# Kernel tuning notes

Measured on AMD Instinct MI355X. Metric: run time of the kernel, lower is better.

## Reference

```python
import jax, jax.numpy as jnp
import numpy as np

N_NODES, N_EDGES = 1024, 4096
D_NODE, D_EDGE, HEADS, N_CLASSES = 128, 256, 4, 16


def setup_inputs() -> dict:
    key = jax.random.key(0)
    ks = jax.random.split(key, 32)
    def w(i, shape):
        return jax.random.normal(ks[i], shape, dtype=jnp.float32) * 0.02
    inp = {
        'node_features': jax.random.normal(ks[0], (N_NODES, D_NODE), dtype=jnp.float32),
        'edge_features': jax.random.normal(ks[1], (N_EDGES, D_EDGE), dtype=jnp.float32),
        'edge_index': jax.random.randint(ks[2], (2, N_EDGES), 0, N_NODES, dtype=jnp.int32),
    }
    i = 3
    for pre in ('a1', 'a2'):
        for nm, shape in [('Wn', (2 * D_NODE, D_EDGE)), ('Wq', (D_EDGE, D_EDGE)),
                          ('Wk', (D_EDGE, D_EDGE)), ('Wv', (D_EDGE, D_EDGE)), ('Wo', (D_EDGE, D_EDGE))]:
            inp[f'{pre}_{nm}'] = w(i, shape); i += 1
            inp[f'{pre}_b{nm[1:].lower()}'] = jnp.zeros((shape[1],), jnp.float32)
    inp['cls_W1'] = w(i, (D_EDGE, D_EDGE)); i += 1
    inp['cls_b1'] = jnp.zeros((D_EDGE,), jnp.float32)
    inp['cls_W2'] = w(i, (D_EDGE, N_CLASSES)); i += 1
    inp['cls_b2'] = jnp.zeros((N_CLASSES,), jnp.float32)
    return inp


def _edge_adjacency(edge_index):
    # edges adjacent iff they share an endpoint (hops=1). [E,E] bool
    src, dst = edge_index[0], edge_index[1]
    return ((src[:, None] == src[None, :]) | (src[:, None] == dst[None, :]) |
            (dst[:, None] == src[None, :]) | (dst[:, None] == dst[None, :]))


def _edge_attention(ef, nf, edge_index, adj, Wn, bn, Wq, bq, Wk, bk, Wv, bv, Wo, bo):
    src, dst = edge_index[0], edge_index[1]
    # gather endpoint node features and fuse into edge representation
    ctx = jnp.concatenate([nf[src], nf[dst]], axis=-1) @ Wn + bn  # [E, D_EDGE]
    x = ef + ctx
    E, D = x.shape
    hd = D // HEADS
    q = (x @ Wq + bq).reshape(E, HEADS, hd)
    k = (x @ Wk + bk).reshape(E, HEADS, hd)
    v = (x @ Wv + bv).reshape(E, HEADS, hd)
    scores = jnp.einsum('ehd,fhd->hef', q, k) / np.float32(np.sqrt(hd))  # [H,E,E]
    scores = jnp.where(adj[None, :, :], scores, jnp.float32(-1e9))
    attn = jax.nn.softmax(scores, axis=-1)
    out = jnp.einsum('hef,fhd->ehd', attn, v).reshape(E, D)
    return x + out @ Wo + bo


def reference(node_features, edge_features, edge_index,
              a1_Wn, a1_bn, a1_Wq, a1_bq, a1_Wk, a1_bk, a1_Wv, a1_bv, a1_Wo, a1_bo,
              a2_Wn, a2_bn, a2_Wq, a2_bq, a2_Wk, a2_bk, a2_Wv, a2_bv, a2_Wo, a2_bo,
              cls_W1, cls_b1, cls_W2, cls_b2):
    adj = _edge_adjacency(edge_index)
    ef = _edge_attention(edge_features, node_features, edge_index, adj,
                         a1_Wn, a1_bn, a1_Wq, a1_bq, a1_Wk, a1_bk, a1_Wv, a1_bv, a1_Wo, a1_bo)
    ef = _edge_attention(ef, node_features, edge_index, adj,
                         a2_Wn, a2_bn, a2_Wq, a2_bq, a2_Wk, a2_bk, a2_Wv, a2_bv, a2_Wo, a2_bo)
    h = jax.nn.gelu(ef @ cls_W1 + cls_b1, approximate=False)
    return h @ cls_W2 + cls_b2
```

## Files before the change

### kernel.cpp

```cpp
#include <hip/hip_runtime.h>
#include <math.h>

#define E_EDGES 4096
#define N_NODES 1024
#define D_NODE 128
#define D_EDGE 256
#define HEADS 4
#define HD 64
#define N_CLASSES 16
#define CAP 128

typedef __attribute__((ext_vector_type(8))) short short8v;
typedef __attribute__((ext_vector_type(4))) short short4v;
typedef __attribute__((ext_vector_type(4))) float f32x4;

__device__ __forceinline__ unsigned short f2bf(float f) {
    unsigned u = __float_as_uint(f);
    return (unsigned short)((u + 0x7FFFu + ((u >> 16) & 1u)) >> 16);
}
__device__ __forceinline__ float bf2f(unsigned short b) {
    return __uint_as_float(((unsigned)b) << 16);
}

__device__ __forceinline__ void gload_lds16(const void* g, void* l) {
    __builtin_amdgcn_global_load_lds((const __attribute__((address_space(1))) void*)g,
                                     (__attribute__((address_space(3))) void*)l, 16, 0, 0);
}

__device__ __forceinline__ void split_unit(
    char* smem, const float* __restrict__ W, short* __restrict__ ho,
    short* __restrict__ lo, int tile)
{
    float* tl = (float*)smem;
    const int t = threadIdx.x;
    const int k0 = (tile >> 2) * 64, n0 = (tile & 3) * 64;
#pragma unroll
    for (int p = 0; p < 4; ++p) {
        const int kr = (t >> 4) + p * 16;
        const int nc = (t & 15) * 4;
        *(float4*)&tl[kr * 65 + nc] = *(const float4*)&W[(size_t)(k0 + kr) * 256 + n0 + nc];
    }
    __syncthreads();
    const int n = t >> 2, ks = (t & 3) * 16;
    short8v h0, h1, l0, l1;
#pragma unroll
    for (int j = 0; j < 8; ++j) {
        const float x = tl[(ks + j) * 65 + n];
        const unsigned short hb = f2bf(x);
        h0[j] = (short)hb; l0[j] = (short)f2bf(x - bf2f(hb));
    }
#pragma unroll
    for (int j = 0; j < 8; ++j) {
        const float x = tl[(ks + 8 + j) * 65 + n];
        const unsigned short hb = f2bf(x);
        h1[j] = (short)hb; l1[j] = (short)f2bf(x - bf2f(hb));
    }
    *(short8v*)&ho[(size_t)(n0 + n) * 256 + k0 + ks] = h0;
    *(short8v*)&ho[(size_t)(n0 + n) * 256 + k0 + ks + 8] = h1;
    *(short8v*)&lo[(size_t)(n0 + n) * 256 + k0 + ks] = l0;
    *(short8v*)&lo[(size_t)(n0 + n) * 256 + k0 + ks + 8] = l1;
}

__device__ __forceinline__ void adj_unit(
    const int* __restrict__ src, const int* __restrict__ dst,
    int* __restrict__ cand, int* __restrict__ ccount, int e, int lane)
{
    const int a = src[e], b = dst[e];
    int* my = cand + (size_t)e * CAP;
    int base = 0;
    for (int c0 = 0; c0 < E_EDGES; c0 += 64) {
        const int f = c0 + lane;
        const int sf = src[f], df = dst[f];
        const bool adj = (sf == a) | (sf == b) | (df == a) | (df == b);
        const unsigned long long mk = __ballot(adj);
        if (adj) {
            const int pos = base + __popcll(mk & ((1ull << lane) - 1ull));
            if (pos < CAP) my[pos] = f;
        }
        base += __popcll(mk);
    }
    if (lane == 0) ccount[e] = (base < CAP) ? base : CAP;
}

__device__ __forceinline__ void mcore32(
    char* smem,
    const float* __restrict__ A, const float* __restrict__ A2,
    const short* __restrict__ BhiT, const short* __restrict__ BloT,
    const float* __restrict__ bias, const float* __restrict__ res,
    const float* __restrict__ res2, float* __restrict__ C,
    int m0, int n0,
    const float* __restrict__ nf, const int* __restrict__ src,
    const int* __restrict__ dst, int act)
{
    short* AsH = (short*)smem;
    short* AsL = (short*)(smem + 5120);
    short* BsH = (short*)(smem + 10240);
    short* BsL = (short*)(smem + 18432);
    const int t = threadIdx.x;
    const int w = t >> 6, lane = t & 63, lr = lane & 15, lg = lane >> 4;
    const int WR = (w >> 1) * 16, WC = (w & 1) * 32;
    const int ar = t >> 3, akc = (t & 7) * 4;
    const int bn = t >> 2, bkc = (t & 3) * 8;

    int nS = 0, nD = 0;
    if (nf) { nS = src[m0 + ar]; nD = dst[m0 + ar]; }

    f32x4 acc0 = {0.f, 0.f, 0.f, 0.f}, acc1 = {0.f, 0.f, 0.f, 0.f};
    float4 av;

#define LOADA_R(k0)                                                            \
    do {                                                                       \
        const int kq = (k0) + akc;                                             \
        if (nf) {                                                              \
            const float* pp = (kq < D_NODE)                                    \
                ? &nf[(size_t)nS * D_NODE + kq]                                \
                : &nf[(size_t)nD * D_NODE + kq - D_NODE];                      \
            av = *(const float4*)pp;                                           \
        } else {                                                               \
            av = *(const float4*)&A[(size_t)(m0 + ar) * 256 + kq];             \
            if (A2) {                                                          \
                const float4 c_ = *(const float4*)&A2[(size_t)(m0 + ar) * 256 + kq]; \
                av.x += c_.x; av.y += c_.y; av.z += c_.z; av.w += c_.w;        \
            }                                                                  \
        }                                                                      \
    } while (0)
#define STOREA_S(buf)                                                          \
    do {                                                                       \
        short4v ah, al;                                                        \
        const float fv[4] = {av.x, av.y, av.z, av.w};                          \
        _Pragma("unroll") for (int j = 0; j < 4; ++j) {                        \
            const unsigned short hb = f2bf(fv[j]);                             \
            ah[j] = (short)hb; al[j] = (short)f2bf(fv[j] - bf2f(hb));          \
        }                                                                      \
        *(short4v*)&AsH[(buf) * 1280 + ar * 40 + akc] = ah;                    \
        *(short4v*)&AsL[(buf) * 1280 + ar * 40 + akc] = al;                    \
    } while (0)
#define STAGE_B(buf, k0)                                                       \
    do {                                                                       \
        gload_lds16(&BhiT[(size_t)(n0 + bn) * 256 + (k0) + bkc],               \
                    BsH + (buf) * 2048 + t * 8);                               \
        gload_lds16(&BloT[(size_t)(n0 + bn) * 256 + (k0) + bkc],               \
                    BsL + (buf) * 2048 + t * 8);                               \
    } while (0)
#define MFMA_STEP(buf)                                                         \
    do {                                                                       \
        const int c0 = WC + lr, c1 = WC + 16 + lr;                             \
        const short8v bH0 = *(const short8v*)&BsH[(buf) * 2048 + c0 * 32 + lg * 8]; \
        const short8v bL0 = *(const short8v*)&BsL[(buf) * 2048 + c0 * 32 + lg * 8]; \
        const short8v bH1 = *(const short8v*)&BsH[(buf) * 2048 + c1 * 32 + lg * 8]; \
        const short8v bL1 = *(const short8v*)&BsL[(buf) * 2048 + c1 * 32 + lg * 8]; \
        const short8v aH = *(const short8v*)&AsH[(buf) * 1280 + (WR + lr) * 40 + lg * 8]; \
        const short8v aL = *(const short8v*)&AsL[(buf) * 1280 + (WR + lr) * 40 + lg * 8]; \
        acc0 = __builtin_amdgcn_mfma_f32_16x16x32_bf16(aH, bH0, acc0, 0, 0, 0);\
        acc1 = __builtin_amdgcn_mfma_f32_16x16x32_bf16(aH, bH1, acc1, 0, 0, 0);\
        acc0 = __builtin_amdgcn_mfma_f32_16x16x32_bf16(aH, bL0, acc0, 0, 0, 0);\
        acc1 = __builtin_amdgcn_mfma_f32_16x16x32_bf16(aH, bL1, acc1, 0, 0, 0);\
        acc0 = __builtin_amdgcn_mfma_f32_16x16x32_bf16(aL, bH0, acc0, 0, 0, 0);\
        acc1 = __builtin_amdgcn_mfma_f32_16x16x32_bf16(aL, bH1, acc1, 0, 0, 0);\
    } while (0)

    LOADA_R(0);
    STAGE_B(0, 0);
    STOREA_S(0);
    __syncthreads();

    for (int kt = 0; kt < 8; ++kt) {
        const int cur = kt & 1;
        if (kt < 7) {
            STAGE_B(cur ^ 1, (kt + 1) * 32);
            LOADA_R((kt + 1) * 32);
        }
        MFMA_STEP(cur);
        if (kt < 7) STOREA_S(cur ^ 1);
        __syncthreads();
    }

#define EPI(accv, ct)                                                          \
    do {                                                                       \
        const int col = n0 + WC + (ct) * 16 + lr;                              \
        const float bb = bias ? bias[col] : 0.f;                               \
        _Pragma("unroll") for (int i = 0; i < 4; ++i) {                        \
            const int row = m0 + WR + lg * 4 + i;                              \
            float v = accv[i] + bb;                                            \
            if (res)  v += res[(size_t)row * D_EDGE + col];                    \
            if (res2) v += res2[(size_t)row * D_EDGE + col];                   \
            if (act == 1) v = 0.5f * v * (1.f + erff(v * 0.70710678118654752f)); \
            C[(size_t)row * D_EDGE + col] = v;                                 \
        }                                                                      \
    } while (0)
    EPI(acc0, 0); EPI(acc1, 1);
#undef LOADA_R
#undef STOREA_S
#undef STAGE_B
#undef MFMA_STEP
#undef EPI
}

__global__ __launch_bounds__(256) void adj_prep(
    const int* __restrict__ src, const int* __restrict__ dst,
    int* __restrict__ cand, int* __restrict__ ccount,
    const float* Wn1, const float* Wn2, short* hiT, short* loT)
{
    __shared__ __attribute__((aligned(16))) char smem[16640];
    if (blockIdx.x < 1024) {
        const int t = threadIdx.x;
        adj_unit(src, dst, cand, ccount, blockIdx.x * 4 + (t >> 6), t & 63);
    } else {
        const int u = blockIdx.x - 1024;
        const int mat = (u >> 4) ? 5 : 0;
        split_unit(smem, (u >> 4) ? Wn2 : Wn1,
                   hiT + (size_t)mat * 65536, loT + (size_t)mat * 65536, u & 15);
    }
}

__global__ __launch_bounds__(256) void ctx_prep(
    const float* __restrict__ nf, const int* __restrict__ src,
    const int* __restrict__ dst, short* hiT, short* loT,
    const float* __restrict__ bn1, const float* __restrict__ bn2,
    float* __restrict__ ctx,
    const float* Wq1, const float* Wk1, const float* Wv1, const float* Wo1,
    const float* Wq2, const float* Wk2, const float* Wv2, const float* Wo2,
    const float* Wc1)
{
    __shared__ __attribute__((aligned(16))) char smem[26624];
    if (blockIdx.x < 1024) {
        const int lid = blockIdx.x;
        const int g = lid & 7, s = lid >> 3;
        const int rowt = g * 32 + (s >> 2);
        const int ct = s & 3;
        const int R = rowt * 32;
        const int Lyr = R >> 12;
        const int r = R & (E_EDGES - 1);
        mcore32(smem, nullptr, nullptr,
                hiT + (size_t)(Lyr * 5) * 65536, loT + (size_t)(Lyr * 5) * 65536,
                Lyr ? bn2 : bn1, nullptr, nullptr,
                ctx + (size_t)Lyr * E_EDGES * D_EDGE,
                r, ct * 64, nf, src, dst, 0);
    } else {
        const int u = blockIdx.x - 1024;
        const int mi = u >> 4;
        const int matIdx[9] = {1, 2, 3, 4, 6, 7, 8, 9, 10};
        const float* Ws[9] = {Wq1, Wk1, Wv1, Wo1, Wq2, Wk2, Wv2, Wo2, Wc1};
        const int mat = matIdx[mi];
        split_unit(smem, Ws[mi], hiT + (size_t)mat * 65536,
                   loT + (size_t)mat * 65536, u & 15);
    }
}

__global__ __launch_bounds__(256) void gemm_qkv32(
    const float* __restrict__ ef_in, const float* __restrict__ ctx,
    const short* __restrict__ whiT, const short* __restrict__ wloT,
    const float* __restrict__ bq, const float* __restrict__ bk,
    const float* __restrict__ bv,
    float* __restrict__ qb, float* __restrict__ kb, float* __restrict__ vb,
    int wbase)
{
    __shared__ __attribute__((aligned(16))) char smem[26624];
    const int lid = blockIdx.x;
    const int g = lid & 7, s = lid >> 3;
    const int rowt = g * 16 + s / 12;
    const int rem = s % 12, wsel = rem >> 2, ct = rem & 3;
    const short* BH = whiT + (size_t)(wbase + 1 + wsel) * 65536;
    const short* BL = wloT + (size_t)(wbase + 1 + wsel) * 65536;
    const float* bias = (wsel == 0) ? bq : (wsel == 1) ? bk : bv;
    float* C = (wsel == 0) ? qb : (wsel == 1) ? kb : vb;
    mcore32(smem, ef_in, ctx, BH, BL, bias, nullptr, nullptr, C,
            rowt * 32, ct * 64, nullptr, nullptr, nullptr, 0);
}

__global__ __launch_bounds__(256) void gemm_g32(
    const float* __restrict__ A, const short* __restrict__ BhiT,
    const short* __restrict__ BloT, const float* __restrict__ bias,
    const float* __restrict__ res, const float* __restrict__ res2,
    float* __restrict__ C, int act)
{
    __shared__ __attribute__((aligned(16))) char smem[26624];
    const int lid = blockIdx.x;
    const int g = lid & 7, s = lid >> 3;
    const int rowt = g * 16 + (s >> 2);
    const int ct = s & 3;
    mcore32(smem, A, nullptr, BhiT, BloT, bias, res, res2, C,
            rowt * 32, ct * 64, nullptr, nullptr, nullptr, act);
}

__global__ __launch_bounds__(256) void attn_sparse5(
    const float* __restrict__ q, const float* __restrict__ k,
    const float* __restrict__ v, const int* __restrict__ cand,
    const int* __restrict__ ccount, float* __restrict__ out)
{
    __shared__ int lc[4][CAP];
    const int t = threadIdx.x;
    const int w = t >> 6, lane = t & 63;
    const int e = blockIdx.x * 4 + w;
    const int h = lane >> 4, il = lane & 15;
    const int m = ccount[e];
    for (int i = lane; i < m; i += 64) lc[w][i] = cand[(size_t)e * CAP + i];

    const float4 q4 = *(const float4*)&q[(size_t)e * D_EDGE + h * HD + il * 4];
    float M = -1e30f, L = 0.f;
    float4 O = make_float4(0.f, 0.f, 0.f, 0.f);

    int i = 0;
    for (; i + 2 <= m; i += 2) {
        const int f0 = lc[w][i], f1 = lc[w][i + 1];
        const float4 k0 = *(const float4*)&k[(size_t)f0 * D_EDGE + h * HD + il * 4];
        const float4 v0 = *(const float4*)&v[(size_t)f0 * D_EDGE + h * HD + il * 4];
        const float4 k1 = *(const float4*)&k[(size_t)f1 * D_EDGE + h * HD + il * 4];
        const float4 v1 = *(const float4*)&v[(size_t)f1 * D_EDGE + h * HD + il * 4];
        float s0 = q4.x * k0.x + q4.y * k0.y + q4.z * k0.z + q4.w * k0.w;
        float s1 = q4.x * k1.x + q4.y * k1.y + q4.z * k1.z + q4.w * k1.w;
        s0 += __shfl_xor(s0, 1); s1 += __shfl_xor(s1, 1);
        s0 += __shfl_xor(s0, 2); s1 += __shfl_xor(s1, 2);
        s0 += __shfl_xor(s0, 4); s1 += __shfl_xor(s1, 4);
        s0 += __shfl_xor(s0, 8); s1 += __shfl_xor(s1, 8);
        s0 *= 0.125f; s1 *= 0.125f;
        const float Mn = fmaxf(M, fmaxf(s0, s1));
        const float al = __expf(M - Mn);
        const float p0 = __expf(s0 - Mn), p1 = __expf(s1 - Mn);
        O.x = O.x * al + p0 * v0.x + p1 * v1.x;
        O.y = O.y * al + p0 * v0.y + p1 * v1.y;
        O.z = O.z * al + p0 * v0.z + p1 * v1.z;
        O.w = O.w * al + p0 * v0.w + p1 * v1.w;
        L = L * al + p0 + p1;
        M = Mn;
    }
    if (i < m) {
        const int f = lc[w][i];
        const float4 kv = *(const float4*)&k[(size_t)f * D_EDGE + h * HD + il * 4];
        const float4 vv = *(const float4*)&v[(size_t)f * D_EDGE + h * HD + il * 4];
        float s = q4.x * kv.x + q4.y * kv.y + q4.z * kv.z + q4.w * kv.w;
        s += __shfl_xor(s, 1);
        s += __shfl_xor(s, 2);
        s += __shfl_xor(s, 4);
        s += __shfl_xor(s, 8);
        s *= 0.125f;
        const float Mn = fmaxf(M, s);
        const float al = __expf(M - Mn);
        const float p = __expf(s - Mn);
        O.x = O.x * al + p * vv.x;
        O.y = O.y * al + p * vv.y;
        O.z = O.z * al + p * vv.z;
        O.w = O.w * al + p * vv.w;
        L = L * al + p;
        M = Mn;
    }
    const float invL = 1.f / L;
    float4 r = make_float4(O.x * invL, O.y * invL, O.z * invL, O.w * invL);
    *(float4*)&out[(size_t)e * D_EDGE + h * HD + il * 4] = r;
}

__global__ __launch_bounds__(256) void cls_out(
    const float* __restrict__ h, const float* __restrict__ W2,
    const float* __restrict__ b2, float* __restrict__ outp)
{
    __shared__ __attribute__((aligned(16))) float W2s[256 * 16];
    const int t = threadIdx.x;
    const int w = t >> 6, lane = t & 63, lr = lane & 15, lg = lane >> 4;
    const int m0 = blockIdx.x * 16;
#pragma unroll
    for (int p = 0; p < 4; ++p) {
        const int idx = t + 256 * p;
        gload_lds16(&W2[(size_t)idx * 4], W2s + (size_t)idx * 4);
    }
    __syncthreads();
    if (w == 0) {
        f32x4 o = {0.f, 0.f, 0.f, 0.f};
#pragma unroll
        for (int kk = 0; kk < 8; ++kk) {
            const float4 h0 = *(const float4*)&h[(size_t)(m0 + lr) * 256 + kk * 32 + lg * 8];
            const float4 h1 = *(const float4*)&h[(size_t)(m0 + lr) * 256 + kk * 32 + lg * 8 + 4];
            short8v aH, aL;
            const float fv[8] = {h0.x, h0.y, h0.z, h0.w, h1.x, h1.y, h1.z, h1.w};
#pragma unroll
            for (int j = 0; j < 8; ++j) {
                const unsigned short hb = f2bf(fv[j]);
                aH[j] = (short)hb; aL[j] = (short)f2bf(fv[j] - bf2f(hb));
            }
            short8v bH, bL;
#pragma unroll
            for (int j = 0; j < 8; ++j) {
                const float x = W2s[(size_t)(kk * 32 + lg * 8 + j) * 16 + lr];
                const unsigned short hb = f2bf(x);
                bH[j] = (short)hb; bL[j] = (short)f2bf(x - bf2f(hb));
            }
            o = __builtin_amdgcn_mfma_f32_16x16x32_bf16(aH, bH, o, 0, 0, 0);
            o = __builtin_amdgcn_mfma_f32_16x16x32_bf16(aH, bL, o, 0, 0, 0);
            o = __builtin_amdgcn_mfma_f32_16x16x32_bf16(aL, bH, o, 0, 0, 0);
        }
#pragma unroll
        for (int i = 0; i < 4; ++i) {
            const int row = m0 + lg * 4 + i;
            outp[(size_t)row * 16 + lr] = o[i] + b2[lr];
        }
    }
}

extern "C" void kernel_launch(void* const* d_in, const int* in_sizes, int n_in,
                              void* d_out, int out_size, void* d_ws, size_t ws_size,
                              hipStream_t stream)
{
    const float* nf = (const float*)d_in[0];
    const float* ef = (const float*)d_in[1];
    const int* ei = (const int*)d_in[2];
    const int* src = ei;
    const int* dst = ei + E_EDGES;

    const float* a_Wn[2] = {(const float*)d_in[3],  (const float*)d_in[13]};
    const float* a_bn[2] = {(const float*)d_in[4],  (const float*)d_in[14]};
    const float* a_Wq[2] = {(const float*)d_in[5],  (const float*)d_in[15]};
    const float* a_bq[2] = {(const float*)d_in[6],  (const float*)d_in[16]};
    const float* a_Wk[2] = {(const float*)d_in[7],  (const float*)d_in[17]};
    const float* a_bk[2] = {(const float*)d_in[8],  (const float*)d_in[18]};
    const float* a_Wv[2] = {(const float*)d_in[9],  (const float*)d_in[19]};
    const float* a_bv[2] = {(const float*)d_in[10], (const float*)d_in[20]};
    const float* a_Wo[2] = {(const float*)d_in[11], (const float*)d_in[21]};
    const float* a_bo[2] = {(const float*)d_in[12], (const float*)d_in[22]};
    const float* cls_W1 = (const float*)d_in[23];
    const float* cls_b1 = (const float*)d_in[24];
    const float* cls_W2 = (const float*)d_in[25];
    const float* cls_b2 = (const float*)d_in[26];

    const size_t buf = (size_t)E_EDGES * D_EDGE;
    float* ws = (float*)d_ws;
    float* ctx1 = ws + 0 * buf;
    float* ctx2 = ws + 1 * buf;
    float* qb   = ws + 2 * buf;
    float* kb   = ws + 3 * buf;
    float* vb   = ws + 4 * buf;
    float* ao   = ws + 5 * buf;
    float* y1   = ws + 6 * buf;
    float* y2   = ctx1;
    float* hb   = qb;
    int* cand   = (int*)(ws + 7 * buf);
    int* ccount = cand + (size_t)E_EDGES * CAP;
    short* whiT = (short*)(ccount + E_EDGES);
    short* wloT = whiT + (size_t)11 * 65536;

    adj_prep<<<1056, 256, 0, stream>>>(src, dst, cand, ccount,
                                       a_Wn[0], a_Wn[1], whiT, wloT);
    ctx_prep<<<1168, 256, 0, stream>>>(nf, src, dst, whiT, wloT,
                                       a_bn[0], a_bn[1], ctx1,
                                       a_Wq[0], a_Wk[0], a_Wv[0], a_Wo[0],
                                       a_Wq[1], a_Wk[1], a_Wv[1], a_Wo[1],
                                       cls_W1);

    const float* ef_in = ef;
    const float* ctxL[2] = {ctx1, ctx2};
    float* yout[2] = {y1, y2};
    for (int L = 0; L < 2; ++L) {
        const int wbase = L * 5;
        gemm_qkv32<<<1536, 256, 0, stream>>>(
            ef_in, ctxL[L], whiT, wloT, a_bq[L], a_bk[L], a_bv[L],
            qb, kb, vb, wbase);
        attn_sparse5<<<E_EDGES / 4, 256, 0, stream>>>(qb, kb, vb, cand, ccount, ao);
        gemm_g32<<<512, 256, 0, stream>>>(
            ao, whiT + (size_t)(wbase + 4) * 65536,
            wloT + (size_t)(wbase + 4) * 65536,
            a_bo[L], ef_in, ctxL[L], yout[L], 0);
        ef_in = yout[L];
    }

    gemm_g32<<<512, 256, 0, stream>>>(
        y2, whiT + (size_t)10 * 65536, wloT + (size_t)10 * 65536,
        cls_b1, nullptr, nullptr, hb, 1);
    cls_out<<<E_EDGES / 16, 256, 0, stream>>>(hb, cls_W2, cls_b2, (float*)d_out);
}
```

Baseline: 123.3 us.

## Fuse classifier GEMMs into one kernel and unroll sparse attention by four

Merges the classifier hidden GEMM with GELU and the output projection into a single kernel. The GELU activations stay in LDS as split bf16 hi/lo, so the fp32 intermediate is never written to or read back from global memory and one launch is removed. Separately, the online-softmax loop in the sparse attention kernel now processes four candidates per iteration instead of two, putting more independent K/V loads in flight. The trade-off is that the fused kernel uses only 256 blocks with 16 rows each and reloads the full W1 tile for every block, and the wider unroll raises register pressure.

```diff
diff --git a/kernel.cpp b/kernel.cpp
--- a/kernel.cpp
+++ b/kernel.cpp
@@ -283,7 +283,7 @@
             rowt * 32, ct * 64, nullptr, nullptr, nullptr, act);
 }
 
-__global__ __launch_bounds__(256) void attn_sparse5(
+__global__ __launch_bounds__(256) void attn_sparse6(
     const float* __restrict__ q, const float* __restrict__ k,
     const float* __restrict__ v, const int* __restrict__ cand,
     const int* __restrict__ ccount, float* __restrict__ out)
@@ -301,30 +301,43 @@
     float4 O = make_float4(0.f, 0.f, 0.f, 0.f);
 
     int i = 0;
-    for (; i + 2 <= m; i += 2) {
+    for (; i + 4 <= m; i += 4) {
         const int f0 = lc[w][i], f1 = lc[w][i + 1];
+        const int f2 = lc[w][i + 2], f3 = lc[w][i + 3];
         const float4 k0 = *(const float4*)&k[(size_t)f0 * D_EDGE + h * HD + il * 4];
         const float4 v0 = *(const float4*)&v[(size_t)f0 * D_EDGE + h * HD + il * 4];
         const float4 k1 = *(const float4*)&k[(size_t)f1 * D_EDGE + h * HD + il * 4];
         const float4 v1 = *(const float4*)&v[(size_t)f1 * D_EDGE + h * HD + il * 4];
+        const float4 k2 = *(const float4*)&k[(size_t)f2 * D_EDGE + h * HD + il * 4];
+        const float4 v2 = *(const float4*)&v[(size_t)f2 * D_EDGE + h * HD + il * 4];
+        const float4 k3 = *(const float4*)&k[(size_t)f3 * D_EDGE + h * HD + il * 4];
+        const float4 v3 = *(const float4*)&v[(size_t)f3 * D_EDGE + h * HD + il * 4];
         float s0 = q4.x * k0.x + q4.y * k0.y + q4.z * k0.z + q4.w * k0.w;
         float s1 = q4.x * k1.x + q4.y * k1.y + q4.z * k1.z + q4.w * k1.w;
+        float s2 = q4.x * k2.x + q4.y * k2.y + q4.z * k2.z + q4.w * k2.w;
+        float s3 = q4.x * k3.x + q4.y * k3.y + q4.z * k3.z + q4.w * k3.w;
         s0 += __shfl_xor(s0, 1); s1 += __shfl_xor(s1, 1);
+        s2 += __shfl_xor(s2, 1); s3 += __shfl_xor(s3, 1);
         s0 += __shfl_xor(s0, 2); s1 += __shfl_xor(s1, 2);
+        s2 += __shfl_xor(s2, 2); s3 += __shfl_xor(s3, 2);
         s0 += __shfl_xor(s0, 4); s1 += __shfl_xor(s1, 4);
+        s2 += __shfl_xor(s2, 4); s3 += __shfl_xor(s3, 4);
         s0 += __shfl_xor(s0, 8); s1 += __shfl_xor(s1, 8);
-        s0 *= 0.125f; s1 *= 0.125f;
-        const float Mn = fmaxf(M, fmaxf(s0, s1));
+        s2 += __shfl_xor(s2, 8); s3 += __shfl_xor(s3, 8);
+        s0 *= 0.125f; s1 *= 0.125f; s2 *= 0.125f; s3 *= 0.125f;
+        const float m01 = fmaxf(s0, s1), m23 = fmaxf(s2, s3);
+        const float Mn = fmaxf(M, fmaxf(m01, m23));
         const float al = __expf(M - Mn);
         const float p0 = __expf(s0 - Mn), p1 = __expf(s1 - Mn);
-        O.x = O.x * al + p0 * v0.x + p1 * v1.x;
-        O.y = O.y * al + p0 * v0.y + p1 * v1.y;
-        O.z = O.z * al + p0 * v0.z + p1 * v1.z;
-        O.w = O.w * al + p0 * v0.w + p1 * v1.w;
-        L = L * al + p0 + p1;
+        const float p2 = __expf(s2 - Mn), p3 = __expf(s3 - Mn);
+        O.x = O.x * al + p0 * v0.x + p1 * v1.x + p2 * v2.x + p3 * v3.x;
+        O.y = O.y * al + p0 * v0.y + p1 * v1.y + p2 * v2.y + p3 * v3.y;
+        O.z = O.z * al + p0 * v0.z + p1 * v1.z + p2 * v2.z + p3 * v3.z;
+        O.w = O.w * al + p0 * v0.w + p1 * v1.w + p2 * v2.w + p3 * v3.w;
+        L = L * al + (p0 + p1) + (p2 + p3);
         M = Mn;
     }
-    if (i < m) {
+    for (; i < m; ++i) {
         const int f = lc[w][i];
         const float4 kv = *(const float4*)&k[(size_t)f * D_EDGE + h * HD + il * 4];
         const float4 vv = *(const float4*)&v[(size_t)f * D_EDGE + h * HD + il * 4];
@@ -349,44 +362,102 @@
     *(float4*)&out[(size_t)e * D_EDGE + h * HD + il * 4] = r;
 }
 
-__global__ __launch_bounds__(256) void cls_out(
-    const float* __restrict__ h, const float* __restrict__ W2,
-    const float* __restrict__ b2, float* __restrict__ outp)
-{
-    __shared__ __attribute__((aligned(16))) float W2s[256 * 16];
+__global__ __launch_bounds__(256) void gemm_cls(
+    const float* __restrict__ y, const short* __restrict__ BhiT,
+    const short* __restrict__ BloT, const float* __restrict__ b1,
+    const float* __restrict__ W2, const float* __restrict__ b2,
+    float* __restrict__ outp)
+{
+    __shared__ __attribute__((aligned(16))) char smem[35840];
+    short* AsH = (short*)smem;
+    short* AsL = (short*)(smem + 1280);
+    short* BsH = (short*)(smem + 2560);
+    short* BsL = (short*)(smem + 18944);
+    short* hH  = (short*)smem;
+    short* hL  = (short*)(smem + 8448);
+    float* W2s = (float*)(smem + 16896);
+
     const int t = threadIdx.x;
     const int w = t >> 6, lane = t & 63, lr = lane & 15, lg = lane >> 4;
     const int m0 = blockIdx.x * 16;
+
+    f32x4 acc[4];
+#pragma unroll
+    for (int ct = 0; ct < 4; ++ct) acc[ct] = (f32x4){0.f, 0.f, 0.f, 0.f};
+
+    for (int kt = 0; kt < 8; ++kt) {
+        const int k0 = kt * 32;
+        if (t < 128) {
+            const int row = t >> 3, kc = (t & 7) * 4;
+            const float4 a4 = *(const float4*)&y[(size_t)(m0 + row) * 256 + k0 + kc];
+            const float fv[4] = {a4.x, a4.y, a4.z, a4.w};
+#pragma unroll
+            for (int j = 0; j < 4; ++j) {
+                const unsigned short hb = f2bf(fv[j]);
+                AsH[row * 40 + kc + j] = (short)hb;
+                AsL[row * 40 + kc + j] = (short)f2bf(fv[j] - bf2f(hb));
+            }
+        }
+#pragma unroll
+        for (int p = 0; p < 4; ++p) {
+            const int idx = t + 256 * p;
+            const int n = idx >> 2, k8 = (idx & 3) * 8;
+            gload_lds16(&BhiT[(size_t)n * 256 + k0 + k8], BsH + (size_t)idx * 8);
+            gload_lds16(&BloT[(size_t)n * 256 + k0 + k8], BsL + (size_t)idx * 8);
+        }
+        __syncthreads();
+        const short8v aH = *(const short8v*)&AsH[lr * 40 + lg * 8];
+        const short8v aL = *(const short8v*)&AsL[lr * 40 + lg * 8];
+#pragma unroll
+        for (int ct = 0; ct < 4; ++ct) {
+            const int c = w * 64 + ct * 16 + lr;
+            const short8v bH = *(const short8v*)&BsH[c * 32 + lg * 8];
+            const short8v bL = *(const short8v*)&BsL[c * 32 + lg * 8];
+            acc[ct] = __builtin_amdgcn_mfma_f32_16x16x32_bf16(aH, bH, acc[ct], 0, 0, 0);
+            acc[ct] = __builtin_amdgcn_mfma_f32_16x16x32_bf16(aH, bL, acc[ct], 0, 0, 0);
+            acc[ct] = __builtin_amdgcn_mfma_f32_16x16x32_bf16(aL, bH, acc[ct], 0, 0, 0);
+        }
+        __syncthreads();
+    }
+
+#pragma unroll
+    for (int ct = 0; ct < 4; ++ct) {
+        const int col = w * 64 + ct * 16 + lr;
+        const float bb = b1[col];
+#pragma unroll
+        for (int i = 0; i < 4; ++i) {
+            const int row = lg * 4 + i;
+            float vv = acc[ct][i] + bb;
+            vv = 0.5f * vv * (1.f + erff(vv * 0.70710678118654752f));
+            const unsigned short hb = f2bf(vv);
+            hH[row * 264 + col] = (short)hb;
+            hL[row * 264 + col] = (short)f2bf(vv - bf2f(hb));
+        }
+    }
 #pragma unroll
     for (int p = 0; p < 4; ++p) {
         const int idx = t + 256 * p;
         gload_lds16(&W2[(size_t)idx * 4], W2s + (size_t)idx * 4);
     }
     __syncthreads();
+
+    f32x4 o = {0.f, 0.f, 0.f, 0.f};
+#pragma unroll
+    for (int kk = 0; kk < 8; ++kk) {
+        const short8v aH = *(const short8v*)&hH[lr * 264 + kk * 32 + lg * 8];
+        const short8v aL = *(const short8v*)&hL[lr * 264 + kk * 32 + lg * 8];
+        short8v bH, bL;
+#pragma unroll
+        for (int j = 0; j < 8; ++j) {
+            const float x = W2s[(size_t)(kk * 32 + lg * 8 + j) * 16 + lr];
+            const unsigned short hb = f2bf(x);
+            bH[j] = (short)hb; bL[j] = (short)f2bf(x - bf2f(hb));
+        }
+        o = __builtin_amdgcn_mfma_f32_16x16x32_bf16(aH, bH, o, 0, 0, 0);
+        o = __builtin_amdgcn_mfma_f32_16x16x32_bf16(aH, bL, o, 0, 0, 0);
+        o = __builtin_amdgcn_mfma_f32_16x16x32_bf16(aL, bH, o, 0, 0, 0);
+    }
     if (w == 0) {
-        f32x4 o = {0.f, 0.f, 0.f, 0.f};
-#pragma unroll
-        for (int kk = 0; kk < 8; ++kk) {
-            const float4 h0 = *(const float4*)&h[(size_t)(m0 + lr) * 256 + kk * 32 + lg * 8];
-            const float4 h1 = *(const float4*)&h[(size_t)(m0 + lr) * 256 + kk * 32 + lg * 8 + 4];
-            short8v aH, aL;
-            const float fv[8] = {h0.x, h0.y, h0.z, h0.w, h1.x, h1.y, h1.z, h1.w};
-#pragma unroll
-            for (int j = 0; j < 8; ++j) {
-                const unsigned short hb = f2bf(fv[j]);
-                aH[j] = (short)hb; aL[j] = (short)f2bf(fv[j] - bf2f(hb));
-            }
-            short8v bH, bL;
-#pragma unroll
-            for (int j = 0; j < 8; ++j) {
-                const float x = W2s[(size_t)(kk * 32 + lg * 8 + j) * 16 + lr];
-                const unsigned short hb = f2bf(x);
-                bH[j] = (short)hb; bL[j] = (short)f2bf(x - bf2f(hb));
-            }
-            o = __builtin_amdgcn_mfma_f32_16x16x32_bf16(aH, bH, o, 0, 0, 0);
-            o = __builtin_amdgcn_mfma_f32_16x16x32_bf16(aH, bL, o, 0, 0, 0);
-            o = __builtin_amdgcn_mfma_f32_16x16x32_bf16(aL, bH, o, 0, 0, 0);
-        }
 #pragma unroll
         for (int i = 0; i < 4; ++i) {
             const int row = m0 + lg * 4 + i;
@@ -430,7 +501,6 @@
     float* ao   = ws + 5 * buf;
     float* y1   = ws + 6 * buf;
     float* y2   = ctx1;
-    float* hb   = qb;
     int* cand   = (int*)(ws + 7 * buf);
     int* ccount = cand + (size_t)E_EDGES * CAP;
     short* whiT = (short*)(ccount + E_EDGES);
@@ -452,7 +522,7 @@
         gemm_qkv32<<<1536, 256, 0, stream>>>(
             ef_in, ctxL[L], whiT, wloT, a_bq[L], a_bk[L], a_bv[L],
             qb, kb, vb, wbase);
-        attn_sparse5<<<E_EDGES / 4, 256, 0, stream>>>(qb, kb, vb, cand, ccount, ao);
+        attn_sparse6<<<E_EDGES / 4, 256, 0, stream>>>(qb, kb, vb, cand, ccount, ao);
         gemm_g32<<<512, 256, 0, stream>>>(
             ao, whiT + (size_t)(wbase + 4) * 65536,
             wloT + (size_t)(wbase + 4) * 65536,
@@ -460,8 +530,7 @@
         ef_in = yout[L];
     }
 
-    gemm_g32<<<512, 256, 0, stream>>>(
+    gemm_cls<<<E_EDGES / 16, 256, 0, stream>>>(
         y2, whiT + (size_t)10 * 65536, wloT + (size_t)10 * 65536,
-        cls_b1, nullptr, nullptr, hb, 1);
-    cls_out<<<E_EDGES / 16, 256, 0, stream>>>(hb, cls_W2, cls_b2, (float*)d_out);
-}
+        cls_b1, cls_W2, cls_b2, (float*)d_out);
+}
```

Measured after the change: 127.0 us (median of 2 runs). 2.9% more time.
